# Optimization experiments

Measured on AMD Instinct MI355X. Metric: run time of the kernel, lower is better.

## Reference

```python
import jax, jax.numpy as jnp
import numpy as np

COST_CLASS, COST_OBJECTNESS, COST_GIOU, COST_CENTER = 1.0, 0.5, 2.0, 1.0
B, Q, G, C = 32, 4096, 32, 128


def setup_inputs() -> dict:
    key = jax.random.key(0)
    ks = jax.random.split(key, 6)
    return {
        "sem_cls_prob": jax.random.uniform(ks[0], (B, Q, C), jnp.float32),
        "objectness_prob": jax.random.uniform(ks[1], (B, Q), jnp.float32),
        "center_dist": jax.random.uniform(ks[2], (B, Q, G), jnp.float32),
        "gious": jax.random.uniform(ks[3], (B, Q, G), jnp.float32) * 2.0 - 1.0,  # gIoU in [-1,1]
        "gt_box_sem_cls_label": jax.random.randint(ks[4], (B, G), 0, C).astype(jnp.int64),
        "nactual_gt": jax.random.randint(ks[5], (B,), 1, G + 1).astype(jnp.int64),
    }


def _lsa(Cmat):
    """Jonker-Volgenant shortest augmenting path Hungarian.
    Cmat: [n, m] float64 with n <= m. Returns p: [m+1] int64, p[j] = row matched
    to column j (or -1), index m is the virtual start column. Equivalent to
    scipy.optimize.linear_sum_assignment on Cmat (modulo ties)."""
    n, m = Cmat.shape
    u = np.zeros(n, np.float64)
    v = np.zeros(m + 1, np.float64)
    p = np.full(m + 1, -1, np.int64)
    way = np.zeros(m, np.int64)
    for i in range(n):
        p[m] = i
        j0 = m
        minv = np.full(m, np.inf)
        used = np.zeros(m + 1, bool)
        while True:
            used[j0] = True
            i0 = p[j0]
            cur = Cmat[i0] - u[i0] - v[:m]            # vectorized Dijkstra relaxation
            better = (~used[:m]) & (cur < minv)
            minv = np.where(better, cur, minv)
            way = np.where(better, j0, way)
            mv = np.where(used[:m], np.inf, minv)
            j1 = int(np.argmin(mv))
            delta = mv[j1]
            rows = p[used]                            # matched rows of used cols (distinct)
            u[rows] += delta
            v[used] -= delta
            minv = np.where(used[:m], minv, minv - delta)
            j0 = j1
            if p[j0] == -1:
                break
        while j0 != m:                                # augment along the path
            j1 = way[j0]
            p[j0] = p[j1]
            j0 = j1
    return p


def hungarian_assign(final_cost, nactual_gt):
    """final_cost: np [B,Q,G]; emulates the per-batch scipy loop of the module."""
    Bn, Qn, _ = final_cost.shape
    per_prop = np.zeros((Bn, Qn), np.int64)
    mask = np.zeros((Bn, Qn), np.float32)
    for b in range(Bn):
        ng = int(nactual_gt[b])
        if ng > 0:
            p = _lsa(final_cost[b, :, :ng].T.astype(np.float64))  # [ng, Q]
            cols = np.nonzero(p[:Qn] >= 0)[0]
            per_prop[b, cols] = p[cols]
            mask[b, cols] = 1.0
    return per_prop, mask


def build_cost(sem_cls_prob, objectness_prob, center_dist, gious, gt_box_sem_cls_label):
    Bn, Qn, _ = sem_cls_prob.shape
    Gn = gt_box_sem_cls_label.shape[1]
    idx = jnp.broadcast_to(gt_box_sem_cls_label[:, None, :], (Bn, Qn, Gn))
    class_mat = -jnp.take_along_axis(sem_cls_prob, idx, axis=2)        # [B,Q,G]
    return (COST_CLASS * class_mat
            - COST_OBJECTNESS * objectness_prob[:, :, None]
            + COST_CENTER * center_dist
            - COST_GIOU * gious)


def reference(sem_cls_prob, objectness_prob, center_dist, gious, gt_box_sem_cls_label, nactual_gt):
    final_cost = build_cost(sem_cls_prob, objectness_prob, center_dist, gious, gt_box_sem_cls_label)
    cost_np = np.asarray(jax.device_get(final_cost))
    per_prop, mask = hungarian_assign(cost_np, np.asarray(jax.device_get(nactual_gt)))
    return jnp.asarray(per_prop), jnp.asarray(mask)
```

## Files before the change

### kernel.cpp

```cpp
#include <hip/hip_runtime.h>
#include <math.h>

#define NB   32
#define BQ   4096
#define GMAX 32
#define NC   128
#define BS   512
#define CPT  (BQ / BS)
#define NWAVE (BS / 64)

#define BBS  256

__launch_bounds__(BBS)
__global__ void build_cost_kernel(const float* __restrict__ sem,
                                  const float* __restrict__ objp,
                                  const float* __restrict__ cent,
                                  const float* __restrict__ giou,
                                  const int*   __restrict__ labels,
                                  const int*   __restrict__ nact,
                                  float* __restrict__ cost)
{
    const int b = blockIdx.x >> 4;
    const int q = ((blockIdx.x & 15) << 8) + threadIdx.x;
    const int ng = nact[b];

    int lab[GMAX];
#pragma unroll
    for (int i = 0; i < GMAX; i++) lab[i] = labels[b * GMAX + i];

    const float*  semrow = sem + ((size_t)b * BQ + q) * NC;
    const float4* cq = (const float4*)(cent + ((size_t)b * BQ + q) * GMAX);
    const float4* gq = (const float4*)(giou + ((size_t)b * BQ + q) * GMAX);

    float4 cr[8], gr[8];
#pragma unroll
    for (int x = 0; x < 8; x++) { cr[x] = cq[x]; gr[x] = gq[x]; }
    float sv[GMAX];
#pragma unroll
    for (int i = 0; i < GMAX; i++) sv[i] = semrow[lab[i]];
    const float ho = __fmul_rn(0.5f, objp[b * BQ + q]);

    const float* crf = (const float*)cr;
    const float* grf = (const float*)gr;
    float* cb = cost + (size_t)b * GMAX * BQ + q;

#pragma unroll
    for (int i = 0; i < GMAX; i++) {
        float c = __fsub_rn(__fadd_rn(__fsub_rn(-sv[i], ho), crf[i]),
                            __fmul_rn(2.0f, grf[i]));
        if (i < ng) cb[(size_t)i * BQ] = c;
    }
}

__launch_bounds__(BS, 1)
__global__ void matcher_kernel(const float* __restrict__ cost,
                               const int*   __restrict__ nact,
                               float* __restrict__ out)
{
    const int b    = blockIdx.x;
    const int tid  = threadIdx.x;
    const int m    = BQ;
    const int wave = tid >> 6;
    const int lane = tid & 63;

    __shared__ __align__(16) short p_lds[BQ + 8];
    __shared__ __align__(16) unsigned short way_lds[BQ];
    __shared__ double u_lds[GMAX];
    __shared__ double   redv[2][NWAVE];
    __shared__ unsigned redpk[2][NWAVE];
    __shared__ int    step_i0[GMAX + 2];
    __shared__ double step_D[GMAX + 2];
    __shared__ float  rmin_v[GMAX];
    __shared__ int    rmin_j[GMAX];
    __shared__ int    unmatched[GMAX];
    __shared__ int    s_nunm;

    for (int k = tid; k < BQ + 8; k += BS) p_lds[k] = -1;
    const int ng = nact[b];
    const float* cb = cost + (size_t)b * GMAX * BQ;
    __syncthreads();

    for (int r = wave; r < ng; r += NWAVE) {
        const float4* row4 = (const float4*)(cb + (size_t)r * BQ);
        float bv = INFINITY; int bj = 0;
#pragma unroll
        for (int it = 0; it < 16; it++) {
            float4 vv = row4[lane + 64 * it];
            int j = (lane + 64 * it) * 4;
            if (vv.x < bv) { bv = vv.x; bj = j; }
            if (vv.y < bv) { bv = vv.y; bj = j + 1; }
            if (vv.z < bv) { bv = vv.z; bj = j + 2; }
            if (vv.w < bv) { bv = vv.w; bj = j + 3; }
        }
#pragma unroll
        for (int off = 32; off >= 1; off >>= 1) {
            float ov = __shfl_down(bv, off, 64);
            int   oj = __shfl_down(bj, off, 64);
            if (ov < bv || (ov == bv && oj < bj)) { bv = ov; bj = oj; }
        }
        if (lane == 0) { rmin_v[r] = bv; rmin_j[r] = bj; }
    }
    __syncthreads();

    if (tid < ng) u_lds[tid] = (double)rmin_v[tid];
    if (tid == 0) {
        int nu = 0;
        for (int i = 0; i < ng; i++) {
            int j = rmin_j[i];
            if (p_lds[j] < 0) p_lds[j] = (short)i;
            else unmatched[nu++] = i;
        }
        s_nunm = nu;
    }
    __syncthreads();
    const int nunm = s_nunm;

    const double INF = (double)INFINITY;
    const int jbase = tid * CPT;
    const float4* cb4 = (const float4*)cb;

    double v_reg[CPT], minv[CPT], enterD[CPT];
    int way_reg[CPT], p_reg[CPT];
#pragma unroll
    for (int k = 0; k < CPT; k++) { v_reg[k] = 0.0; way_reg[k] = m; enterD[k] = 0.0; }

    for (int t = 0; t < nunm; t++) {
        const int ri = unmatched[t];

        int4 pv = ((const int4*)p_lds)[tid];
        p_reg[0] = (int)(short)(pv.x & 0xFFFF); p_reg[1] = pv.x >> 16;
        p_reg[2] = (int)(short)(pv.y & 0xFFFF); p_reg[3] = pv.y >> 16;
        p_reg[4] = (int)(short)(pv.z & 0xFFFF); p_reg[5] = pv.z >> 16;
        p_reg[6] = (int)(short)(pv.w & 0xFFFF); p_reg[7] = pv.w >> 16;

        const float4* r4 = cb4 + (size_t)ri * (BQ / 4) + tid * 2;
        float4 c0 = r4[0];
        float4 c1 = r4[1];
        double ui0 = u_lds[ri];

#pragma unroll
        for (int k = 0; k < CPT; k++) minv[k] = INF;
        unsigned used_mask = 0;
        int i0 = ri, j0 = m, ns = 0, buf = 0, jfin;
        double D = 0.0;

        while (true) {
            float cf[CPT] = {c0.x, c0.y, c0.z, c0.w, c1.x, c1.y, c1.z, c1.w};

            double bestv = INF;
            unsigned bestpk = ((unsigned)m << 8);
#pragma unroll
            for (int k = 0; k < CPT; k++) {
                bool un = !((used_mask >> k) & 1u);
                double cur = ((double)cf[k] - ui0) - v_reg[k];
                bool better = un && (cur < minv[k]);
                if (better) { minv[k] = cur; way_reg[k] = j0; }
                double mv = un ? minv[k] : INF;
                if (mv < bestv) {
                    bestv = mv;
                    bestpk = (((unsigned)(jbase + k)) << 8) | (unsigned)(p_reg[k] + 1);
                }
            }

#pragma unroll
            for (int off = 32; off >= 1; off >>= 1) {
                double   ov  = __shfl_down(bestv, off, 64);
                unsigned opk = __shfl_down(bestpk, off, 64);
                if (ov < bestv || (ov == bestv && opk < bestpk)) { bestv = ov; bestpk = opk; }
            }
            if (lane == 0) { redv[buf][wave] = bestv; redpk[buf][wave] = bestpk; }
            __syncthreads();

            double delta = redv[buf][0]; unsigned pk = redpk[buf][0];
#pragma unroll
            for (int w = 1; w < NWAVE; w++) {
                double ov = redv[buf][w]; unsigned opk = redpk[buf][w];
                if (ov < delta || (ov == delta && opk < pk)) { delta = ov; pk = opk; }
            }
            const int j1 = (int)(pk >> 8);
            const int pi = (int)(pk & 0xFFu) - 1;

            if (tid == 0) { step_i0[ns] = i0; step_D[ns] = D; }
            D += delta;
            ns++;

            if (pi < 0) { jfin = j1; break; }

            const float4* n4 = cb4 + (size_t)pi * (BQ / 4) + tid * 2;
            c0 = n4[0];
            c1 = n4[1];
            ui0 = u_lds[pi];

#pragma unroll
            for (int k = 0; k < CPT; k++)
                if (!((used_mask >> k) & 1u)) minv[k] -= delta;

            unsigned kk = (unsigned)(j1 - jbase);
            if (kk < CPT) { used_mask |= (1u << kk); enterD[kk] = D; }

            i0 = pi; j0 = j1; buf ^= 1;
        }

#pragma unroll
        for (int k = 0; k < CPT; k++)
            if ((used_mask >> k) & 1u) v_reg[k] -= (D - enterD[k]);

        int4 wv;
        wv.x = (way_reg[0] & 0xFFFF) | (way_reg[1] << 16);
        wv.y = (way_reg[2] & 0xFFFF) | (way_reg[3] << 16);
        wv.z = (way_reg[4] & 0xFFFF) | (way_reg[5] << 16);
        wv.w = (way_reg[6] & 0xFFFF) | (way_reg[7] << 16);
        ((int4*)way_lds)[tid] = wv;

        __syncthreads();
        if (tid < ns) u_lds[step_i0[tid]] += D - step_D[tid];
        if (tid == 0) {
            int jc = jfin;
            while (jc != m) {
                int jp = (int)way_lds[jc];
                p_lds[jc] = (jp == m) ? (short)ri : p_lds[jp];
                jc = jp;
            }
        }
        __syncthreads();
    }

#pragma unroll
    for (int k = 0; k < CPT; k++) {
        int j = jbase + k;
        short pj = p_lds[j];
        out[(size_t)b * BQ + j] = (pj >= 0) ? (float)pj : 0.0f;
        out[(size_t)NB * BQ + (size_t)b * BQ + j] = (pj >= 0) ? 1.0f : 0.0f;
    }
}

extern "C" void kernel_launch(void* const* d_in, const int* in_sizes, int n_in,
                              void* d_out, int out_size, void* d_ws, size_t ws_size,
                              hipStream_t stream) {
    const float* sem    = (const float*)d_in[0];
    const float* objp   = (const float*)d_in[1];
    const float* cent   = (const float*)d_in[2];
    const float* giou   = (const float*)d_in[3];
    const int*   labels = (const int*)d_in[4];
    const int*   nact   = (const int*)d_in[5];
    float* out  = (float*)d_out;
    float* cost = (float*)d_ws;

    build_cost_kernel<<<NB * 16, BBS, 0, stream>>>(sem, objp, cent, giou,
                                                   labels, nact, cost);
    matcher_kernel<<<NB, BS, 0, stream>>>(cost, nact, out);
}
```

Baseline: 155.4 us.

## Fuse per-row minimum partials into cost build and reshape build grid

The cost-build kernel now gives each 64-thread wave a 64-query tile and 8 GT rows. It does a wave-level argmin per row and writes partial (min, index) pairs to a workspace buffer. The matcher then reduces 64 partials per row instead of rescanning the full 4096-column cost row, which removes a serial pre-pass from the single-block-per-batch matcher. Blocks whose rows are all beyond nactual_gt now exit early. The cost is extra shuffles in the build kernel and a workspace offset at 16 MB that assumes enough workspace.

```diff
diff --git a/kernel.cpp b/kernel.cpp
--- a/kernel.cpp
+++ b/kernel.cpp
@@ -8,53 +8,75 @@
 #define BS   512
 #define CPT  (BQ / BS)
 #define NWAVE (BS / 64)
-
-#define BBS  256
-
-__launch_bounds__(BBS)
+#define NT64 (BQ / 64)
+
+__launch_bounds__(256, 6)
 __global__ void build_cost_kernel(const float* __restrict__ sem,
                                   const float* __restrict__ objp,
                                   const float* __restrict__ cent,
                                   const float* __restrict__ giou,
                                   const int*   __restrict__ labels,
                                   const int*   __restrict__ nact,
-                                  float* __restrict__ cost)
+                                  float* __restrict__ cost,
+                                  float2* __restrict__ rowpart)
 {
-    const int b = blockIdx.x >> 4;
-    const int q = ((blockIdx.x & 15) << 8) + threadIdx.x;
-    const int ng = nact[b];
-
-    int lab[GMAX];
-#pragma unroll
-    for (int i = 0; i < GMAX; i++) lab[i] = labels[b * GMAX + i];
+    const int blk  = blockIdx.x;
+    const int b    = blk >> 6;
+    const int qt   = blk & 63;
+    const int lane = threadIdx.x & 63;
+    const int quad = threadIdx.x >> 6;
+    const int q    = (qt << 6) + lane;
+    const int r0   = quad << 3;
+    const int ng   = nact[b];
+
+    if (r0 >= ng) return;
+
+    int lab[8];
+#pragma unroll
+    for (int k = 0; k < 8; k++) lab[k] = labels[b * GMAX + r0 + k];
 
     const float*  semrow = sem + ((size_t)b * BQ + q) * NC;
-    const float4* cq = (const float4*)(cent + ((size_t)b * BQ + q) * GMAX);
-    const float4* gq = (const float4*)(giou + ((size_t)b * BQ + q) * GMAX);
-
-    float4 cr[8], gr[8];
-#pragma unroll
-    for (int x = 0; x < 8; x++) { cr[x] = cq[x]; gr[x] = gq[x]; }
-    float sv[GMAX];
-#pragma unroll
-    for (int i = 0; i < GMAX; i++) sv[i] = semrow[lab[i]];
+    const float4* cq = (const float4*)(cent + ((size_t)b * BQ + q) * GMAX) + (r0 >> 2);
+    const float4* gq = (const float4*)(giou + ((size_t)b * BQ + q) * GMAX) + (r0 >> 2);
+
+    float4 cr[2], gr[2];
+    cr[0] = cq[0]; cr[1] = cq[1];
+    gr[0] = gq[0]; gr[1] = gq[1];
+    float sv[8];
+#pragma unroll
+    for (int k = 0; k < 8; k++) sv[k] = semrow[lab[k]];
     const float ho = __fmul_rn(0.5f, objp[b * BQ + q]);
 
     const float* crf = (const float*)cr;
     const float* grf = (const float*)gr;
-    float* cb = cost + (size_t)b * GMAX * BQ + q;
-
-#pragma unroll
-    for (int i = 0; i < GMAX; i++) {
-        float c = __fsub_rn(__fadd_rn(__fsub_rn(-sv[i], ho), crf[i]),
-                            __fmul_rn(2.0f, grf[i]));
-        if (i < ng) cb[(size_t)i * BQ] = c;
+    float* cb = cost + ((size_t)b * GMAX + r0) * BQ + q;
+
+#pragma unroll
+    for (int k = 0; k < 8; k++) {
+        const int i = r0 + k;
+        if (i < ng) {
+            float c = __fsub_rn(__fadd_rn(__fsub_rn(-sv[k], ho), crf[k]),
+                                __fmul_rn(2.0f, grf[k]));
+            cb[(size_t)k * BQ] = c;
+
+            float bv = c; int bj = q;
+#pragma unroll
+            for (int off = 32; off >= 1; off >>= 1) {
+                float ov = __shfl_down(bv, off, 64);
+                int   oj = __shfl_down(bj, off, 64);
+                if (ov < bv || (ov == bv && oj < bj)) { bv = ov; bj = oj; }
+            }
+            if (lane == 0)
+                rowpart[((size_t)b * GMAX + i) * NT64 + qt] =
+                    make_float2(bv, __int_as_float(bj));
+        }
     }
 }
 
 __launch_bounds__(BS, 1)
-__global__ void matcher_kernel(const float* __restrict__ cost,
-                               const int*   __restrict__ nact,
+__global__ void matcher_kernel(const float*  __restrict__ cost,
+                               const float2* __restrict__ rowpart,
+                               const int*    __restrict__ nact,
                                float* __restrict__ out)
 {
     const int b    = blockIdx.x;
@@ -81,17 +103,8 @@
     __syncthreads();
 
     for (int r = wave; r < ng; r += NWAVE) {
-        const float4* row4 = (const float4*)(cb + (size_t)r * BQ);
-        float bv = INFINITY; int bj = 0;
-#pragma unroll
-        for (int it = 0; it < 16; it++) {
-            float4 vv = row4[lane + 64 * it];
-            int j = (lane + 64 * it) * 4;
-            if (vv.x < bv) { bv = vv.x; bj = j; }
-            if (vv.y < bv) { bv = vv.y; bj = j + 1; }
-            if (vv.z < bv) { bv = vv.z; bj = j + 2; }
-            if (vv.w < bv) { bv = vv.w; bj = j + 3; }
-        }
+        float2 pp = (rowpart + ((size_t)b * GMAX + r) * NT64)[lane];
+        float bv = pp.x; int bj = __float_as_int(pp.y);
 #pragma unroll
         for (int off = 32; off >= 1; off >>= 1) {
             float ov = __shfl_down(bv, off, 64);
@@ -244,9 +257,10 @@
     const int*   labels = (const int*)d_in[4];
     const int*   nact   = (const int*)d_in[5];
     float* out  = (float*)d_out;
-    float* cost = (float*)d_ws;
-
-    build_cost_kernel<<<NB * 16, BBS, 0, stream>>>(sem, objp, cent, giou,
-                                                   labels, nact, cost);
-    matcher_kernel<<<NB, BS, 0, stream>>>(cost, nact, out);
+    float*  cost    = (float*)d_ws;
+    float2* rowpart = (float2*)((char*)d_ws + (size_t)16 * 1024 * 1024);
+
+    build_cost_kernel<<<NB * NT64, 256, 0, stream>>>(sem, objp, cent, giou,
+                                                     labels, nact, cost, rowpart);
+    matcher_kernel<<<NB, BS, 0, stream>>>(cost, rowpart, nact, out);
 }
```

After: 146.0 us. 1.06x faster.
